# Kernel tuning notes

Measured on AMD Instinct MI355X. Metric: run time of the kernel, lower is better.

## Reference

```python
import jax, jax.numpy as jnp
import numpy as np

B, L, D_IN, D_OUT = 4, 1024, 2048, 2048
H, G = 32, 8            # num_heads, num_kv_groups
HD = D_OUT // H         # head_dim = 64
R = H // G              # group_size = 4


def setup_inputs() -> dict:
    key = jax.random.key(0)
    ks = jax.random.split(key, 7)
    s = 0.02
    return {
        "query": jax.random.normal(ks[0], (B, L, D_IN), jnp.float32),
        "key": jax.random.normal(ks[1], (B, L, D_IN), jnp.float32),
        "value": jax.random.normal(ks[2], (B, L, D_IN), jnp.float32),
        "Wq": jax.random.normal(ks[3], (D_IN, D_OUT), jnp.float32) * s,
        "Wk": jax.random.normal(ks[4], (D_IN, G * HD), jnp.float32) * s,
        "Wv": jax.random.normal(ks[5], (D_IN, G * HD), jnp.float32) * s,
        "Wo": jax.random.normal(ks[6], (D_OUT, D_OUT), jnp.float32) * s,
        # causal mask: positions where mask==True are set to -inf (original uses attn_mask == 1)
        "attn_mask": jnp.triu(jnp.ones((L, L), dtype=bool), k=1),
    }


def reference(query, key, value, Wq, Wk, Wv, Wo, attn_mask):
    b, t, _ = query.shape
    # projections (Linear, no bias)
    q = (query @ Wq).reshape(b, t, G, R, HD)      # head h = g*R + r matches repeat_interleave ordering
    k = (key @ Wk).reshape(b, -1, G, HD)
    v = (value @ Wv).reshape(b, -1, G, HD)
    # NOTE: original code applies NO 1/sqrt(head_dim) scaling — kept faithful.
    # scores: (b, g, r, t, s); KV broadcast over r instead of repeat_interleave
    scores = jnp.einsum('btgrd,bsgd->bgrts', q, k)
    scores = jnp.where(attn_mask[None, None, None, :, :], -jnp.inf, scores)
    weights = jax.nn.softmax(scores, axis=-1)     # dropout p=0.0 -> identity
    ctx = jnp.einsum('bgrts,bsgd->btgrd', weights, v).reshape(b, t, D_OUT)
    attn_output = ctx @ Wo
    attn_output_weights = weights.reshape(b * H, t, -1)  # (b n) t s
    return attn_output, attn_output_weights
```

## Files before the change

kernel.cpp:

```cpp
#include <hip/hip_runtime.h>
#include <math.h>

typedef _Float16 f16;
typedef __attribute__((ext_vector_type(8))) _Float16 f16x8;
typedef __attribute__((ext_vector_type(4))) _Float16 f16x4;
typedef __attribute__((ext_vector_type(4))) float f32x4;
typedef unsigned int u32;

#define MFMA16(a, b, c) __builtin_amdgcn_mfma_f32_16x16x32_f16(a, b, c, 0, 0, 0)

__device__ __forceinline__ void gload16(const void* g, void* l) {
  __builtin_amdgcn_global_load_lds((const __attribute__((address_space(1))) u32*)g,
                                   (__attribute__((address_space(3))) u32*)l, 16, 0, 0);
}

__global__ __launch_bounds__(256) void cast3_kernel(
    const float* __restrict__ q, const float* __restrict__ k, const float* __restrict__ v,
    f16* __restrict__ qh, f16* __restrict__ kh, f16* __restrict__ vh) {
  const int bx = blockIdx.x;
  const int sel = bx >> 13;
  const float* in = (sel == 0) ? q : (sel == 1) ? k : v;
  f16* out = (sel == 0) ? qh : (sel == 1) ? kh : vh;
  const int i = (bx & 8191) * 1024 + threadIdx.x * 4;
  float4 vv = *(const float4*)(in + i);
  f16x4 h;
  h[0] = (f16)vv.x; h[1] = (f16)vv.y; h[2] = (f16)vv.z; h[3] = (f16)vv.w;
  *(f16x4*)(out + i) = h;
}

__global__ __launch_bounds__(256) void transpose4_kernel(
    const float* __restrict__ Wq, const float* __restrict__ Wk,
    const float* __restrict__ Wv, const float* __restrict__ Wo,
    f16* __restrict__ WqT, f16* __restrict__ WkT,
    f16* __restrict__ WvT, f16* __restrict__ WoT) {
  __shared__ f16 tile[64][66];
  int bx = blockIdx.x;
  const float* in;
  f16* out;
  int K, N, id;
  if (bx < 1024)      { in = Wq; out = WqT; K = 2048; N = 2048; id = bx; }
  else if (bx < 1280) { in = Wk; out = WkT; K = 2048; N = 512;  id = bx - 1024; }
  else if (bx < 1536) { in = Wv; out = WvT; K = 2048; N = 512;  id = bx - 1280; }
  else                { in = Wo; out = WoT; K = 2048; N = 2048; id = bx - 1536; }
  const int ntn = N >> 6;
  const int tk = (id / ntn) * 64, tn = (id % ntn) * 64;
  const int t = threadIdx.x;
#pragma unroll
  for (int i = 0; i < 16; i++) {
    int idx = i * 256 + t;
    int r = idx >> 6, c = idx & 63;
    tile[c][r] = (f16)in[(size_t)(tk + r) * N + tn + c];
  }
  __syncthreads();
#pragma unroll
  for (int i = 0; i < 16; i++) {
    int idx = i * 256 + t;
    int r = idx >> 6, c = idx & 63;
    out[(size_t)(tn + r) * K + tk + c] = tile[r][c];
  }
}

template <bool F32OUT>
__device__ __forceinline__ void gemm_body(const f16* __restrict__ Ap,
                                          const f16* __restrict__ Btp,
                                          void* __restrict__ Cp,
                                          int m0, int n0, int N, int K, int vmode) {
  const int tid = threadIdx.x, lane = tid & 63, wid = tid >> 6;
  const int lg = lane >> 4, lr = lane & 15;
  const int wr = (wid >> 1) << 6, wc = (wid & 1) << 6;
  __shared__ f16 As[2][128 * 64];
  __shared__ f16 Bs[2][128 * 64];
  auto stage = [&](const f16* Gp, f16* Ls, int row0, int k0) {
#pragma unroll
    for (int c = 0; c < 4; c++) {
      int u = c * 256 + tid;
      int row = u >> 3, slot = u & 7;
      int gs = slot ^ (row & 7);
      gload16(Gp + (size_t)(row0 + row) * K + k0 + gs * 8,
              Ls + (c * 256 + wid * 64) * 8);
    }
  };
  f32x4 acc[4][4] = {};
  const int nk = K >> 6;
  stage(Ap, As[0], m0, 0);
  stage(Btp, Bs[0], n0, 0);
  for (int k = 0; k < nk; k++) {
    const int cb = k & 1;
    __builtin_amdgcn_s_barrier();
    __builtin_amdgcn_sched_barrier(0);
    if (k + 1 < nk) {
      stage(Ap, As[cb ^ 1], m0, (k + 1) << 6);
      stage(Btp, Bs[cb ^ 1], n0, (k + 1) << 6);
      __builtin_amdgcn_sched_barrier(0);
      asm volatile("s_waitcnt vmcnt(8)" ::: "memory");
    } else {
      __builtin_amdgcn_sched_barrier(0);
      asm volatile("s_waitcnt vmcnt(0)" ::: "memory");
    }
    __builtin_amdgcn_s_barrier();
    __builtin_amdgcn_sched_barrier(0);
    asm volatile("" ::: "memory");
#pragma unroll
    for (int kk = 0; kk < 2; kk++) {
      f16x8 af[4], bf[4];
#pragma unroll
      for (int i = 0; i < 4; i++) {
        int row = wr + i * 16 + lr;
        int sl = (kk * 4 + lg) ^ (row & 7);
        af[i] = *(const f16x8*)&As[cb][row * 64 + sl * 8];
      }
#pragma unroll
      for (int i = 0; i < 4; i++) {
        int row = wc + i * 16 + lr;
        int sl = (kk * 4 + lg) ^ (row & 7);
        bf[i] = *(const f16x8*)&Bs[cb][row * 64 + sl * 8];
      }
#pragma unroll
      for (int i = 0; i < 4; i++)
#pragma unroll
        for (int j = 0; j < 4; j++)
          acc[i][j] = MFMA16(af[i], bf[j], acc[i][j]);
    }
  }
  if (F32OUT) {
    float* C = (float*)Cp;
#pragma unroll
    for (int i = 0; i < 4; i++)
#pragma unroll
      for (int j = 0; j < 4; j++)
#pragma unroll
        for (int rg = 0; rg < 4; rg++) {
          int row = m0 + wr + i * 16 + lg * 4 + rg;
          int col = n0 + wc + j * 16 + lr;
          C[(size_t)row * N + col] = acc[i][j][rg];
        }
  } else if (vmode) {
    f16* C = (f16*)Cp;
#pragma unroll
    for (int i = 0; i < 4; i++)
#pragma unroll
      for (int j = 0; j < 4; j++)
#pragma unroll
        for (int rg = 0; rg < 4; rg++) {
          int row = m0 + wr + i * 16 + lg * 4 + rg;
          int col = n0 + wc + j * 16 + lr;
          C[((size_t)(row >> 10) * 512 + col) * 1024 + (row & 1023)] = (f16)acc[i][j][rg];
        }
  } else {
    f16* C = (f16*)Cp;
#pragma unroll
    for (int i = 0; i < 4; i++)
#pragma unroll
      for (int j = 0; j < 4; j++)
#pragma unroll
        for (int rg = 0; rg < 4; rg++) {
          int row = m0 + wr + i * 16 + lg * 4 + rg;
          int col = n0 + wc + j * 16 + lr;
          C[(size_t)row * N + col] = (f16)acc[i][j][rg];
        }
  }
}

__global__ __launch_bounds__(256) void gemm_proj(
    const f16* __restrict__ qh, const f16* __restrict__ WqT, f16* __restrict__ Qp,
    const f16* __restrict__ kh, const f16* __restrict__ WkT, f16* __restrict__ Kpj,
    const f16* __restrict__ vh, const f16* __restrict__ WvT, f16* __restrict__ VTp) {
  const int bx = blockIdx.x;
  const f16 *Ap, *Btp;
  f16* Cp;
  int N, nsh, vmode, tile;
  if (bx < 512)      { Ap = qh; Btp = WqT; Cp = Qp;  N = 2048; nsh = 4; vmode = 0; tile = bx; }
  else if (bx < 640) { Ap = kh; Btp = WkT; Cp = Kpj; N = 512;  nsh = 2; vmode = 0; tile = bx - 512; }
  else               { Ap = vh; Btp = WvT; Cp = VTp; N = 512;  nsh = 2; vmode = 1; tile = bx - 640; }
  const int m0 = (tile >> nsh) << 7, n0 = (tile & ((1 << nsh) - 1)) << 7;
  gemm_body<false>(Ap, Btp, (void*)Cp, m0, n0, N, 2048, vmode);
}

__global__ __launch_bounds__(256) void gemm_out(
    const f16* __restrict__ Ap, const f16* __restrict__ Btp, float* __restrict__ Cp) {
  const int tile = blockIdx.x;
  const int m0 = (tile >> 4) << 7, n0 = (tile & 15) << 7;
  gemm_body<true>(Ap, Btp, (void*)Cp, m0, n0, 2048, 2048, 0);
}

__global__ __launch_bounds__(256) void attn_kernel(
    const f16* __restrict__ Qp, const f16* __restrict__ Kp, const f16* __restrict__ VTp,
    float* __restrict__ Wout, f16* __restrict__ Ctx) {
  __shared__ f16 Kt[2][64 * 64];
  __shared__ f16 Vt[2][64 * 64];
  __shared__ f16 Wt[4][32 * 64];
  const int bx = (blockIdx.x & 7) * 128 + (blockIdx.x >> 3);
  const int qt = bx & 31, g = (bx >> 5) & 7, b = bx >> 8;
  const int tid = threadIdx.x, lane = tid & 63, wid = tid >> 6;
  const int lg = lane >> 4, lr = lane & 15;
  const int h = g * 4 + wid;
  const int q0 = qt * 32;
  const int st_max = (q0 + 31) >> 6;
  const float S0 = 12.0f;

  f16x8 aq[2][2];
#pragma unroll
  for (int mi = 0; mi < 2; mi++)
#pragma unroll
    for (int kk = 0; kk < 2; kk++)
      aq[mi][kk] = *(const f16x8*)(Qp + (size_t)(b * 1024 + q0 + mi * 16 + lr) * 2048 +
                                   h * 64 + kk * 32 + lg * 8);

  float l_[2][4] = {};

  auto stageK = [&](int st, int buf) {
#pragma unroll
    for (int c = 0; c < 2; c++) {
      int u = c * 256 + tid;
      int row = u >> 3, slot = u & 7;
      int gs = slot ^ (row & 7);
      gload16(Kp + (size_t)(b * 1024 + st * 64 + row) * 512 + g * 64 + gs * 8,
              &Kt[buf][(c * 256 + wid * 64) * 8]);
    }
  };
  auto stageV = [&](int st, int buf) {
#pragma unroll
    for (int c = 0; c < 2; c++) {
      int u = c * 256 + tid;
      int row = u >> 3, slot = u & 7;
      int gs = slot ^ (row & 7);
      gload16(VTp + ((size_t)b * 512 + g * 64 + row) * 1024 + st * 64 + gs * 8,
              &Vt[buf][(c * 256 + wid * 64) * 8]);
    }
  };

  int cur = 0;
  stageK(0, 0);
  for (int st = 0; st <= st_max; st++) {
    __syncthreads();
    if (st < st_max) {
      stageK(st + 1, cur ^ 1);
    } else {
      stageK(0, cur ^ 1);
      stageV(0, cur ^ 1);
    }
    f16x8 bk[4][2];
#pragma unroll
    for (int ni = 0; ni < 4; ni++)
#pragma unroll
      for (int kk = 0; kk < 2; kk++) {
        int row = ni * 16 + lr;
        int sl = (kk * 4 + lg) ^ (row & 7);
        bk[ni][kk] = *(const f16x8*)&Kt[cur][row * 64 + sl * 8];
      }
#pragma unroll
    for (int mi = 0; mi < 2; mi++) {
      f32x4 s[4];
#pragma unroll
      for (int ni = 0; ni < 4; ni++) {
        f32x4 z = {};
        z = MFMA16(aq[mi][0], bk[ni][0], z);
        z = MFMA16(aq[mi][1], bk[ni][1], z);
        s[ni] = z;
      }
      if (st == st_max) {
#pragma unroll
        for (int ni = 0; ni < 4; ni++)
#pragma unroll
          for (int rg = 0; rg < 4; rg++)
            if (st * 64 + ni * 16 + lr > q0 + mi * 16 + lg * 4 + rg) s[ni][rg] = -INFINITY;
      }
#pragma unroll
      for (int rg = 0; rg < 4; rg++) {
        float rs = __expf(s[0][rg] - S0) + __expf(s[1][rg] - S0) +
                   __expf(s[2][rg] - S0) + __expf(s[3][rg] - S0);
        rs += __shfl_xor(rs, 1);
        rs += __shfl_xor(rs, 2);
        rs += __shfl_xor(rs, 4);
        rs += __shfl_xor(rs, 8);
        l_[mi][rg] += rs;
      }
    }
    cur ^= 1;
  }
#pragma unroll
  for (int i = 0; i < 2; i++)
#pragma unroll
    for (int j = 0; j < 4; j++) l_[i][j] = 1.0f / l_[i][j];

  f32x4 o[2][4] = {};
  for (int st = 0; st <= st_max; st++) {
    __syncthreads();
    if (st < st_max) {
      stageK(st + 1, cur ^ 1);
      stageV(st + 1, cur ^ 1);
    }
    f16x8 bk[4][2];
#pragma unroll
    for (int ni = 0; ni < 4; ni++)
#pragma unroll
      for (int kk = 0; kk < 2; kk++) {
        int row = ni * 16 + lr;
        int sl = (kk * 4 + lg) ^ (row & 7);
        bk[ni][kk] = *(const f16x8*)&Kt[cur][row * 64 + sl * 8];
      }
#pragma unroll
    for (int mi = 0; mi < 2; mi++) {
#pragma unroll
      for (int ni = 0; ni < 4; ni++) {
        f32x4 z = {};
        z = MFMA16(aq[mi][0], bk[ni][0], z);
        z = MFMA16(aq[mi][1], bk[ni][1], z);
#pragma unroll
        for (int rg = 0; rg < 4; rg++) {
          float sv = z[rg];
          if (st == st_max && (st * 64 + ni * 16 + lr > q0 + mi * 16 + lg * 4 + rg))
            sv = -INFINITY;
          float w = __expf(sv - S0) * l_[mi][rg];
          int rowl = mi * 16 + lg * 4 + rg;
          __builtin_nontemporal_store(
              w, &Wout[((size_t)(b * 32 + h) * 1024 + q0 + rowl) * 1024 +
                       st * 64 + ni * 16 + lr]);
          int sl2 = (2 * ni + (lr >> 3)) ^ (rowl & 7);
          Wt[wid][rowl * 64 + sl2 * 8 + (lr & 7)] = (f16)w;
        }
      }
    }
#pragma unroll
    for (int kk = 0; kk < 2; kk++) {
      f16x8 aw[2], bv[4];
#pragma unroll
      for (int i = 0; i < 2; i++) {
        int rw = i * 16 + lr;
        int sl = (kk * 4 + lg) ^ (rw & 7);
        aw[i] = *(const f16x8*)&Wt[wid][rw * 64 + sl * 8];
      }
#pragma unroll
      for (int j = 0; j < 4; j++) {
        int rv = j * 16 + lr;
        int sl = (kk * 4 + lg) ^ (rv & 7);
        bv[j] = *(const f16x8*)&Vt[cur][rv * 64 + sl * 8];
      }
#pragma unroll
      for (int i = 0; i < 2; i++)
#pragma unroll
        for (int j = 0; j < 4; j++)
          o[i][j] = MFMA16(aw[i], bv[j], o[i][j]);
    }
    cur ^= 1;
  }

  {
    f32x4 z4 = {0.f, 0.f, 0.f, 0.f};
    for (int st = st_max + 1; st < 16; st++) {
      size_t base = ((size_t)(b * 32 + h) * 1024 + q0) * 1024 + st * 64;
#pragma unroll
      for (int i = 0; i < 8; i++) {
        int u = i * 64 + lane;
        int row = u >> 4, c4 = u & 15;
        __builtin_nontemporal_store(z4, (f32x4*)(Wout + base + (size_t)row * 1024 + c4 * 4));
      }
    }
  }
#pragma unroll
  for (int i = 0; i < 2; i++)
#pragma unroll
    for (int j = 0; j < 4; j++)
#pragma unroll
      for (int rg = 0; rg < 4; rg++)
        Ctx[(size_t)(b * 1024 + q0 + i * 16 + lg * 4 + rg) * 2048 +
            h * 64 + j * 16 + lr] = (f16)o[i][j][rg];
}

extern "C" void kernel_launch(void* const* d_in, const int* in_sizes, int n_in,
                              void* d_out, int out_size, void* d_ws, size_t ws_size,
                              hipStream_t stream) {
  const float* query = (const float*)d_in[0];
  const float* key   = (const float*)d_in[1];
  const float* value = (const float*)d_in[2];
  const float* Wq    = (const float*)d_in[3];
  const float* Wk    = (const float*)d_in[4];
  const float* Wv    = (const float*)d_in[5];
  const float* Wo    = (const float*)d_in[6];

  float* out0 = (float*)d_out;
  float* wout = out0 + (size_t)4 * 1024 * 2048;

  char* ws = (char*)d_ws;
  size_t off = 0;
  auto alloc = [&](size_t bytes) {
    char* p = ws + off;
    off += (bytes + 255) & ~(size_t)255;
    return p;
  };
  const size_t NT = 4096;
  f16* qh  = (f16*)alloc(NT * 2048 * 2);
  f16* kh  = (f16*)alloc(NT * 2048 * 2);
  f16* vh  = (f16*)alloc(NT * 2048 * 2);
  f16* WqT = (f16*)alloc((size_t)2048 * 2048 * 2);
  f16* WkT = (f16*)alloc((size_t)512 * 2048 * 2);
  f16* WvT = (f16*)alloc((size_t)512 * 2048 * 2);
  f16* WoT = (f16*)alloc((size_t)2048 * 2048 * 2);
  f16* Qp  = (f16*)alloc(NT * 2048 * 2);
  f16* Kpj = (f16*)alloc(NT * 512 * 2);
  f16* VTp = (f16*)alloc(NT * 512 * 2);
  f16* ctx = (f16*)alloc(NT * 2048 * 2);
  (void)ws_size;

  hipLaunchKernelGGL(cast3_kernel, dim3(3 * 8192), dim3(256), 0, stream,
                     query, key, value, qh, kh, vh);
  hipLaunchKernelGGL(transpose4_kernel, dim3(2560), dim3(256), 0, stream,
                     Wq, Wk, Wv, Wo, WqT, WkT, WvT, WoT);
  hipLaunchKernelGGL(gemm_proj, dim3(768), dim3(256), 0, stream,
                     qh, WqT, Qp, kh, WkT, Kpj, vh, WvT, VTp);
  hipLaunchKernelGGL(attn_kernel, dim3(1024), dim3(256), 0, stream,
                     Qp, Kpj, VTp, wout, ctx);
  hipLaunchKernelGGL(gemm_out, dim3(512), dim3(256), 0, stream, ctx, WoT, out0);
  (void)in_sizes; (void)n_in; (void)out_size;
}
```

Baseline: 337.3 us.

## Fuse cast and transpose kernels; zero masked attention weights inside projection GEMM

Merges the input-cast and weight-transpose kernels into one launch. The zero-fill of the fully masked upper-triangle tiles of the attention-weight output moves out of the attention kernel and into extra blocks of the projection GEMM launch, interleaved 3:2 with GEMM tiles. The intent is to overlap the bandwidth-bound zero stores with the compute-bound GEMM and to shorten the attention kernel's tail. The risk is that the zero-store blocks compete with GEMM blocks for memory bandwidth and CU slots.

Measured after the change: 330.2 us. 1.02x faster.

```diff
diff --git a/kernel.cpp b/kernel.cpp
--- a/kernel.cpp
+++ b/kernel.cpp
@@ -14,37 +14,37 @@
                                    (__attribute__((address_space(3))) u32*)l, 16, 0, 0);
 }
 
-__global__ __launch_bounds__(256) void cast3_kernel(
+__global__ __launch_bounds__(256) void prep_kernel(
     const float* __restrict__ q, const float* __restrict__ k, const float* __restrict__ v,
-    f16* __restrict__ qh, f16* __restrict__ kh, f16* __restrict__ vh) {
-  const int bx = blockIdx.x;
-  const int sel = bx >> 13;
-  const float* in = (sel == 0) ? q : (sel == 1) ? k : v;
-  f16* out = (sel == 0) ? qh : (sel == 1) ? kh : vh;
-  const int i = (bx & 8191) * 1024 + threadIdx.x * 4;
-  float4 vv = *(const float4*)(in + i);
-  f16x4 h;
-  h[0] = (f16)vv.x; h[1] = (f16)vv.y; h[2] = (f16)vv.z; h[3] = (f16)vv.w;
-  *(f16x4*)(out + i) = h;
-}
-
-__global__ __launch_bounds__(256) void transpose4_kernel(
+    f16* __restrict__ qh, f16* __restrict__ kh, f16* __restrict__ vh,
     const float* __restrict__ Wq, const float* __restrict__ Wk,
     const float* __restrict__ Wv, const float* __restrict__ Wo,
     f16* __restrict__ WqT, f16* __restrict__ WkT,
     f16* __restrict__ WvT, f16* __restrict__ WoT) {
   __shared__ f16 tile[64][66];
-  int bx = blockIdx.x;
+  const int bx = blockIdx.x;
+  const int t = threadIdx.x;
+  if (bx < 24576) {
+    const int sel = bx >> 13;
+    const float* in = (sel == 0) ? q : (sel == 1) ? k : v;
+    f16* out = (sel == 0) ? qh : (sel == 1) ? kh : vh;
+    const int i = (bx & 8191) * 1024 + t * 4;
+    float4 vv = *(const float4*)(in + i);
+    f16x4 h;
+    h[0] = (f16)vv.x; h[1] = (f16)vv.y; h[2] = (f16)vv.z; h[3] = (f16)vv.w;
+    *(f16x4*)(out + i) = h;
+    return;
+  }
+  int id = bx - 24576;
   const float* in;
   f16* out;
-  int K, N, id;
-  if (bx < 1024)      { in = Wq; out = WqT; K = 2048; N = 2048; id = bx; }
-  else if (bx < 1280) { in = Wk; out = WkT; K = 2048; N = 512;  id = bx - 1024; }
-  else if (bx < 1536) { in = Wv; out = WvT; K = 2048; N = 512;  id = bx - 1280; }
-  else                { in = Wo; out = WoT; K = 2048; N = 2048; id = bx - 1536; }
+  int K, N;
+  if (id < 1024)      { in = Wq; out = WqT; K = 2048; N = 2048; }
+  else if (id < 1280) { in = Wk; out = WkT; K = 2048; N = 512;  id -= 1024; }
+  else if (id < 1536) { in = Wv; out = WvT; K = 2048; N = 512;  id -= 1280; }
+  else                { in = Wo; out = WoT; K = 2048; N = 2048; id -= 1536; }
   const int ntn = N >> 6;
   const int tk = (id / ntn) * 64, tn = (id % ntn) * 64;
-  const int t = threadIdx.x;
 #pragma unroll
   for (int i = 0; i < 16; i++) {
     int idx = i * 256 + t;
@@ -164,14 +164,36 @@
 __global__ __launch_bounds__(256) void gemm_proj(
     const f16* __restrict__ qh, const f16* __restrict__ WqT, f16* __restrict__ Qp,
     const f16* __restrict__ kh, const f16* __restrict__ WkT, f16* __restrict__ Kpj,
-    const f16* __restrict__ vh, const f16* __restrict__ WvT, f16* __restrict__ VTp) {
+    const f16* __restrict__ vh, const f16* __restrict__ WvT, f16* __restrict__ VTp,
+    float* __restrict__ wout) {
   const int bx = blockIdx.x;
+  const int grp = bx / 5, rem = bx % 5;
+  if (rem >= 3) {
+    const int zid = grp * 2 + (rem - 3);
+#pragma unroll
+    for (int ci = 0; ci < 4; ci++) {
+      const int c = zid * 4 + ci;
+      const int bh = c >> 4, k = c & 15;
+      if (k == 15) continue;
+      const int cols0 = (k + 1) << 6;
+      const int nc4 = (1024 - cols0) >> 2;
+      float* base = wout + (size_t)bh * 1024 * 1024 + (size_t)(k << 6) * 1024 + cols0;
+      f32x4 z = {};
+      for (int r = 0; r < 64; r++) {
+        float* rp = base + (size_t)r * 1024;
+        for (int c4 = (int)threadIdx.x; c4 < nc4; c4 += 256)
+          __builtin_nontemporal_store(z, (f32x4*)(rp + c4 * 4));
+      }
+    }
+    return;
+  }
+  const int gid = grp * 3 + rem;
   const f16 *Ap, *Btp;
   f16* Cp;
   int N, nsh, vmode, tile;
-  if (bx < 512)      { Ap = qh; Btp = WqT; Cp = Qp;  N = 2048; nsh = 4; vmode = 0; tile = bx; }
-  else if (bx < 640) { Ap = kh; Btp = WkT; Cp = Kpj; N = 512;  nsh = 2; vmode = 0; tile = bx - 512; }
-  else               { Ap = vh; Btp = WvT; Cp = VTp; N = 512;  nsh = 2; vmode = 1; tile = bx - 640; }
+  if (gid < 512)      { Ap = qh; Btp = WqT; Cp = Qp;  N = 2048; nsh = 4; vmode = 0; tile = gid; }
+  else if (gid < 640) { Ap = kh; Btp = WkT; Cp = Kpj; N = 512;  nsh = 2; vmode = 0; tile = gid - 512; }
+  else                { Ap = vh; Btp = WvT; Cp = VTp; N = 512;  nsh = 2; vmode = 1; tile = gid - 640; }
   const int m0 = (tile >> nsh) << 7, n0 = (tile & ((1 << nsh) - 1)) << 7;
   gemm_body<false>(Ap, Btp, (void*)Cp, m0, n0, N, 2048, vmode);
 }
@@ -345,18 +367,6 @@
     cur ^= 1;
   }
 
-  {
-    f32x4 z4 = {0.f, 0.f, 0.f, 0.f};
-    for (int st = st_max + 1; st < 16; st++) {
-      size_t base = ((size_t)(b * 32 + h) * 1024 + q0) * 1024 + st * 64;
-#pragma unroll
-      for (int i = 0; i < 8; i++) {
-        int u = i * 64 + lane;
-        int row = u >> 4, c4 = u & 15;
-        __builtin_nontemporal_store(z4, (f32x4*)(Wout + base + (size_t)row * 1024 + c4 * 4));
-      }
-    }
-  }
 #pragma unroll
   for (int i = 0; i < 2; i++)
 #pragma unroll
@@ -402,12 +412,11 @@
   f16* ctx = (f16*)alloc(NT * 2048 * 2);
   (void)ws_size;
 
-  hipLaunchKernelGGL(cast3_kernel, dim3(3 * 8192), dim3(256), 0, stream,
-                     query, key, value, qh, kh, vh);
-  hipLaunchKernelGGL(transpose4_kernel, dim3(2560), dim3(256), 0, stream,
+  hipLaunchKernelGGL(prep_kernel, dim3(27136), dim3(256), 0, stream,
+                     query, key, value, qh, kh, vh,
                      Wq, Wk, Wv, Wo, WqT, WkT, WvT, WoT);
-  hipLaunchKernelGGL(gemm_proj, dim3(768), dim3(256), 0, stream,
-                     qh, WqT, Qp, kh, WkT, Kpj, vh, WvT, VTp);
+  hipLaunchKernelGGL(gemm_proj, dim3(1280), dim3(256), 0, stream,
+                     qh, WqT, Qp, kh, WkT, Kpj, vh, WvT, VTp, wout);
   hipLaunchKernelGGL(attn_kernel, dim3(1024), dim3(256), 0, stream,
                      Qp, Kpj, VTp, wout, ctx);
   hipLaunchKernelGGL(gemm_out, dim3(512), dim3(256), 0, stream, ctx, WoT, out0);
```
